# Kernel tuning notes

Measured on AMD Instinct MI355X. Metric: run time of the kernel, lower is better.

The kernel has to match this reference:

```python
import jax, jax.numpy as jnp
import numpy as np

ANCHORS_ALL = np.array([[10.,13.],[16.,30.],[33.,23.],[30.,61.],[62.,45.],
                        [59.,119.],[116.,90.],[156.,198.],[373.,326.]], np.float32)
ANCHORS_MASK = [0, 1, 2]
NUM_CLASS = 80
BBOX_ATTRIB = 5 + NUM_CLASS
IGNORE_THRES = 0.7
EPS = 1e-12


def _iou_cxcywh(a, b):
    ax1, ax2 = a[..., 0] - a[..., 2] / 2, a[..., 0] + a[..., 2] / 2
    ay1, ay2 = a[..., 1] - a[..., 3] / 2, a[..., 1] + a[..., 3] / 2
    bx1, bx2 = b[..., 0] - b[..., 2] / 2, b[..., 0] + b[..., 2] / 2
    by1, by2 = b[..., 1] - b[..., 3] / 2, b[..., 1] + b[..., 3] / 2
    iw = jnp.clip(jnp.minimum(ax2, bx2) - jnp.maximum(ax1, bx1), 0.0)
    ih = jnp.clip(jnp.minimum(ay2, by2) - jnp.maximum(ay1, by1), 0.0)
    inter = iw * ih
    union = a[..., 2] * a[..., 3] + b[..., 2] * b[..., 3] - inter
    return inter / (union + 1e-16)


def _build_targets(pred_boxes, target, anchors_all, anchors, nH, nW):
    # vectorized version of the per-(batch, gt-box) python double loop
    nB, nT, _ = target.shape
    nA = anchors.shape[0]
    # emulate `break` on first all-zero target row via cumulative validity
    valid = jnp.cumprod((target.sum(-1) != 0).astype(jnp.int32), axis=1).astype(bool)  # [B,T]
    gx, gy = target[..., 1] * nW, target[..., 2] * nH
    gw, gh = target[..., 3] * nW, target[..., 4] * nH
    gi = jnp.clip(gx.astype(jnp.int32), 0, nW - 1)
    gj = jnp.clip(gy.astype(jnp.int32), 0, nH - 1)
    gt_boxes = jnp.stack([gx, gy, gw, gh], -1)                                    # [B,T,4]
    # IoU of every GT against every predicted box -> ignore mask for noobj
    ious = _iou_cxcywh(pred_boxes.reshape(nB, 1, -1, 4), gt_boxes[:, :, None, :])  # [B,T,P]
    ignore = (ious > IGNORE_THRES) & valid[..., None]
    noobj_mask = 1.0 - jnp.any(ignore, axis=1).reshape(nB, nA, nH, nW).astype(jnp.float32)
    # anchor matching on w/h only (both boxes centered at origin)
    aw, ah = anchors_all[:, 0], anchors_all[:, 1]                                  # [9]
    inter = jnp.minimum(gw[..., None], aw) * jnp.minimum(gh[..., None], ah)
    union = gw[..., None] * gh[..., None] + aw * ah - inter
    best = jnp.argmax(inter / (union + 1e-16), axis=-1)                            # [B,T]
    lut = -np.ones(len(ANCHORS_ALL), np.int32)
    lut[np.array(ANCHORS_MASK)] = np.arange(nA, dtype=np.int32)
    a_loc = jnp.asarray(lut)[best]
    write = valid & (a_loc >= 0)                # only GTs whose best anchor is in this head's mask
    a_loc = jnp.clip(a_loc, 0)
    b_idx = jnp.where(write, jnp.arange(nB)[:, None], nB)   # route masked-out writes to dummy row nB
    coord_v = jnp.sqrt(2.0 - target[..., 3] * target[..., 4])
    tw_v = jnp.log(gw / anchors[a_loc, 0] + 1e-16)
    th_v = jnp.log(gh / anchors[a_loc, 1] + 1e-16)
    cls_i = jnp.clip(target[..., 0].astype(jnp.int32), 0, NUM_CLASS - 1)

    def scat(vals):
        return jnp.zeros((nB + 1, nA, nH, nW), jnp.float32).at[b_idx, a_loc, gj, gi].set(vals)[:nB]

    obj_mask = scat(jnp.ones_like(gx))
    box_coord_mask = scat(coord_v)
    tx = scat(gx - gi)
    ty = scat(gy - gj)
    tw = scat(tw_v)
    th = scat(th_v)
    tcls = (jnp.zeros((nB + 1, nA, nH, nW, NUM_CLASS), jnp.float32)
            .at[b_idx, a_loc, gj, gi, cls_i].set(1.0)[:nB])
    return obj_mask, noobj_mask, box_coord_mask, obj_mask, tcls, tx, ty, tw, th


def _bce_sum(p, t):
    return -jnp.sum(t * jnp.log(p + EPS) + (1.0 - t) * jnp.log(1.0 - p + EPS))


def _forward(x, target, img_dim):
    nB, _, nH, nW = x.shape
    nA = len(ANCHORS_MASK)
    stride = img_dim / nH
    anchors_all = jnp.asarray(ANCHORS_ALL) / stride
    anchors = anchors_all[jnp.asarray(ANCHORS_MASK)]
    preds = x.reshape(nB, nA, BBOX_ATTRIB, nH, nW).transpose(0, 1, 3, 4, 2)  # [B,A,H,W,85]
    preds_xy = jax.nn.sigmoid(preds[..., :2])
    preds_wh = preds[..., 2:4]
    preds_conf = jax.nn.sigmoid(preds[..., 4])
    preds_cls = jax.nn.sigmoid(preds[..., 5:])
    mesh_xy = jnp.stack(jnp.meshgrid(jnp.arange(nW, dtype=jnp.float32),
                                     jnp.arange(nH, dtype=jnp.float32)), -1)  # [H,W,2] = (x,y)
    # decoded boxes are detached in the original (used only to build targets)
    pred_boxes = jnp.concatenate(
        [jax.lax.stop_gradient(preds_xy) + mesh_xy,
         jnp.exp(jax.lax.stop_gradient(preds_wh)) * anchors[None, :, None, None, :]], -1)
    tgt = jax.lax.stop_gradient(target)  # target.detach() in original
    (obj_mask, noobj_mask, box_coord_mask, tconf, tcls,
     tx, ty, tw, th) = _build_targets(pred_boxes, tgt, anchors_all, anchors, nH, nW)
    mse = lambda a, b: jnp.sum((a - b) ** 2)
    loss_x = mse(preds_xy[..., 0] * box_coord_mask, tx * box_coord_mask) / 2
    loss_y = mse(preds_xy[..., 1] * box_coord_mask, ty * box_coord_mask) / 2
    loss_w = mse(preds_wh[..., 0] * box_coord_mask, tw * box_coord_mask) / 2
    loss_h = mse(preds_wh[..., 1] * box_coord_mask, th * box_coord_mask) / 2
    loss_conf = (_bce_sum(preds_conf * obj_mask, obj_mask)
                 + _bce_sum(preds_conf * noobj_mask, jnp.zeros_like(preds_conf)))
    # BCE over cls entries of object cells only (sum reduction) == mask-weighted sum
    loss_cls = -jnp.sum(obj_mask[..., None] * (tcls * jnp.log(preds_cls + EPS)
                                               + (1.0 - tcls) * jnp.log(1.0 - preds_cls + EPS)))
    return loss_x + loss_y + loss_w + loss_h + loss_conf + loss_cls


def setup_inputs() -> dict:
    key = jax.random.key(0)
    k1, k2, k3, k4 = jax.random.split(key, 4)
    nB, nT = 16, 50
    x = jax.random.normal(k1, (nB, 3 * BBOX_ATTRIB, 76, 76), jnp.float32)
    cls = jnp.floor(jax.random.uniform(k2, (nB, nT, 1)) * NUM_CLASS)
    cxy = jax.random.uniform(k3, (nB, nT, 2), minval=0.05, maxval=0.95)
    wh = jax.random.uniform(k4, (nB, nT, 2), minval=0.02, maxval=0.4)
    target = jnp.concatenate([cls, cxy, wh], -1).astype(jnp.float32)
    return {"x": x, "target": target, "img_dim": 608}


def reference(x, target, img_dim):
    return _forward(x, target, img_dim)
```

## Files before the change

kernel.cpp:

```cpp
#include <hip/hip_runtime.h>

#define NBATCH 16
#define NTGT   50
#define NA     3
#define NH     76
#define NW     76
#define HW     (NH*NW)
#define NC     80
#define NATT   85
#define CELLS  (NA*HW)

__device__ __constant__ float c_anchors[18] = {
  10.f,13.f, 16.f,30.f, 33.f,23.f, 30.f,61.f, 62.f,45.f,
  59.f,119.f, 116.f,90.f, 156.f,198.f, 373.f,326.f };

#define OFF_GX   0
#define OFF_GY   800
#define OFF_GW   1600
#define OFF_GH   2400
#define OFF_TX   3200
#define OFF_TY   4000
#define OFF_TW   4800
#define OFF_TH   5600
#define OFF_CV   6400
#define OFF_WKEY 7200
#define OFF_CLS  8000
#define OFF_NV   8800

__device__ inline float read_dim(const void* p) {
  int iv = *(const int*)p;
  if (iv > 0 && iv < (1 << 24)) return (float)iv;
  return *(const float*)p;
}

__global__ void yolo_prep(const float* __restrict__ tgt,
                          const void*  __restrict__ dimp,
                          float*       __restrict__ wsf) {
  int tid = threadIdx.x;
  int* wsi = (int*)wsf;
  if (tid < NBATCH) wsi[OFF_NV + tid] = NTGT;
  __syncthreads();
  if (tid < NBATCH * NTGT) {
    float stride = read_dim(dimp) / (float)NH;
    float inv_stride = 1.0f / stride;
    int b = tid / NTGT;
    const float* tr = tgt + tid * 5;
    float cls = tr[0], cx = tr[1], cy = tr[2], w = tr[3], h = tr[4];
    float s = cls + cx + cy + w + h;
    if (s == 0.0f) atomicMin(&wsi[OFF_NV + b], tid - b * NTGT);
    float gx = cx * NW, gy = cy * NH, gw = w * NW, gh = h * NH;
    int gi = min(max((int)gx, 0), NW - 1);
    int gj = min(max((int)gy, 0), NH - 1);
    float best_r = -1.0f; int best = 0;
    for (int k = 0; k < 9; k++) {
      float aw = c_anchors[2*k] * inv_stride, ah = c_anchors[2*k+1] * inv_stride;
      float inter = fminf(gw, aw) * fminf(gh, ah);
      float uni   = gw * gh + aw * ah - inter;
      float r = inter / (uni + 1e-16f);
      if (r > best_r) { best_r = r; best = k; }
    }
    int a_loc = (best < NA) ? best : 0;
    int wkey  = (best < NA) ? (a_loc * HW + gj * NW + gi) : -1;
    float aw = c_anchors[2*a_loc] * inv_stride, ah = c_anchors[2*a_loc+1] * inv_stride;
    wsf[OFF_GX + tid] = gx;  wsf[OFF_GY + tid] = gy;
    wsf[OFF_GW + tid] = gw;  wsf[OFF_GH + tid] = gh;
    wsf[OFF_TX + tid] = gx - (float)gi;
    wsf[OFF_TY + tid] = gy - (float)gj;
    wsf[OFF_TW + tid] = logf(gw / aw + 1e-16f);
    wsf[OFF_TH + tid] = logf(gh / ah + 1e-16f);
    wsf[OFF_CV + tid] = sqrtf(2.0f - w * h);
    int ci = (int)cls; ci = min(max(ci, 0), NC - 1);
    wsi[OFF_WKEY + tid] = wkey;
    wsi[OFF_CLS  + tid] = ci;
  }
}

__launch_bounds__(256)
__global__ void yolo_main(const float* __restrict__ x,
                          const float* __restrict__ wsf,
                          const void*  __restrict__ dimp,
                          float*       __restrict__ out) {
  __shared__ float sx1[NTGT], sx2[NTGT], sy1[NTGT], sy2[NTGT], sarea[NTGT];
  __shared__ float stx[NTGT], sty[NTGT], stw[NTGT], sth[NTGT], scv[NTGT];
  __shared__ int   swkey[NTGT], scls[NTGT];
  __shared__ int   snv;
  __shared__ float sred[4];

  int b   = blockIdx.y;
  int tid = threadIdx.x;
  if (tid < NTGT) {
    int g = b * NTGT + tid;
    float gx = wsf[OFF_GX+g], gy = wsf[OFF_GY+g], gw = wsf[OFF_GW+g], gh = wsf[OFF_GH+g];
    sx1[tid] = gx - gw * 0.5f;  sx2[tid] = gx + gw * 0.5f;
    sy1[tid] = gy - gh * 0.5f;  sy2[tid] = gy + gh * 0.5f;
    sarea[tid] = gw * gh;
    stx[tid] = wsf[OFF_TX+g];  sty[tid] = wsf[OFF_TY+g];
    stw[tid] = wsf[OFF_TW+g];  sth[tid] = wsf[OFF_TH+g];
    scv[tid] = wsf[OFF_CV+g];
    const int* wsi = (const int*)wsf;
    swkey[tid] = wsi[OFF_WKEY+g];
    scls[tid]  = wsi[OFF_CLS +g];
  }
  if (tid == 0) snv = ((const int*)wsf)[OFF_NV + b];
  __syncthreads();

  float loss = 0.0f;
  int cell = blockIdx.x * blockDim.x + tid;
  if (cell < CELLS) {
    int a   = cell / HW;
    int rem = cell - a * HW;
    int j   = rem / NW;
    int i   = rem - j * NW;
    const float* xb = x + (size_t)(b * (NA*NATT) + a * NATT) * HW + rem;
    float px = xb[0*HW], py = xb[1*HW], pw = xb[2*HW], ph = xb[3*HW], pc = xb[4*HW];
    float spx   = 1.0f / (1.0f + __expf(-px));
    float spy   = 1.0f / (1.0f + __expf(-py));
    float sconf = 1.0f / (1.0f + __expf(-pc));
    float stride = read_dim(dimp) / (float)NH;
    float aw = c_anchors[2*a] / stride, ah = c_anchors[2*a+1] / stride;
    float bw = __expf(pw) * aw, bh = __expf(ph) * ah;
    float bx = spx + (float)i, by = spy + (float)j;
    float ax1 = bx - bw * 0.5f, ax2 = bx + bw * 0.5f;
    float ay1 = by - bh * 0.5f, ay2 = by + bh * 0.5f;
    float areaA = bw * bh;

    int winner = -1;
    unsigned cb0 = 0, cb1 = 0, cb2 = 0;
    bool ign = false;
    int nv = snv;
    for (int t = 0; t < nv; t++) {
      float iw = fmaxf(fminf(ax2, sx2[t]) - fmaxf(ax1, sx1[t]), 0.0f);
      float ih = fmaxf(fminf(ay2, sy2[t]) - fmaxf(ay1, sy1[t]), 0.0f);
      float inter = iw * ih;
      float iou = inter / (areaA + sarea[t] - inter + 1e-16f);
      ign = ign | (iou > 0.7f);
      if (swkey[t] == cell) {
        winner = t;
        int c = scls[t];
        if (c < 32)      cb0 |= (1u << c);
        else if (c < 64) cb1 |= (1u << (c - 32));
        else             cb2 |= (1u << (c - 64));
      }
    }
    if (!ign) loss += -__logf(1.0f - sconf + 1e-12f);
    if (winner >= 0) {
      loss += -__logf(sconf + 1e-12f);
      float m  = scv[winner];
      float dx = (spx - stx[winner]) * m;
      float dy = (spy - sty[winner]) * m;
      float dw = (pw  - stw[winner]) * m;
      float dh = (ph  - sth[winner]) * m;
      loss += 0.5f * (dx*dx + dy*dy + dw*dw + dh*dh);
      for (int c = 0; c < NC; c++) {
        float pv = 1.0f / (1.0f + __expf(-xb[(5 + c) * HW]));
        bool on = (c < 32) ? ((cb0 >> c) & 1u)
                : (c < 64) ? ((cb1 >> (c - 32)) & 1u)
                           : ((cb2 >> (c - 64)) & 1u);
        loss += on ? -__logf(pv + 1e-12f) : -__logf(1.0f - pv + 1e-12f);
      }
    }
  }

  for (int off = 32; off > 0; off >>= 1) loss += __shfl_down(loss, off, 64);
  int wave = tid >> 6, lane = tid & 63;
  if (lane == 0) sred[wave] = loss;
  __syncthreads();
  if (tid == 0) {
    atomicAdd(out, sred[0] + sred[1] + sred[2] + sred[3]);
  }
}

extern "C" void kernel_launch(void* const* d_in, const int* in_sizes, int n_in,
                              void* d_out, int out_size, void* d_ws, size_t ws_size,
                              hipStream_t stream) {
  const float* x    = (const float*)d_in[0];
  const float* tgt  = (const float*)d_in[1];
  const void*  dimp = d_in[2];
  float* out = (float*)d_out;
  float* wsf = (float*)d_ws;

  hipMemsetAsync(out, 0, sizeof(float) * out_size, stream);

  yolo_prep<<<1, 832, 0, stream>>>(tgt, dimp, wsf);

  dim3 grid((CELLS + 255) / 256, NBATCH);
  yolo_main<<<grid, 256, 0, stream>>>(x, wsf, dimp, out);
}
```

Before: 170.1 us.

## Move object-cell loss into per-batch prep kernel; slim noobj IoU loop

Object-cell loss (box regression and class BCE) now runs in the prep kernel, one thread per GT. Duplicate keys are resolved so that the last GT with a given key wins and class bits are ORed. The per-cell main kernel keeps only the ignore-IoU test and reads packed float4 boxes from shared memory. The division is replaced by a multiply-compare, and the key comparison and bitmask work per cell per target are gone. This reduces the inner-loop instruction count and shared-memory traffic in the main kernel. In exchange, the prep kernel now does the serial 80-class loop for matched targets.

```diff
diff --git a/kernel.cpp b/kernel.cpp
--- a/kernel.cpp
+++ b/kernel.cpp
@@ -14,18 +14,8 @@
   10.f,13.f, 16.f,30.f, 33.f,23.f, 30.f,61.f, 62.f,45.f,
   59.f,119.f, 116.f,90.f, 156.f,198.f, 373.f,326.f };
 
-#define OFF_GX   0
-#define OFF_GY   800
-#define OFF_GW   1600
-#define OFF_GH   2400
-#define OFF_TX   3200
-#define OFF_TY   4000
-#define OFF_TW   4800
-#define OFF_TH   5600
-#define OFF_CV   6400
-#define OFF_WKEY 7200
-#define OFF_CLS  8000
-#define OFF_NV   8800
+#define OFF_AREA 3200
+#define OFF_NV   4000
 
 __device__ inline float read_dim(const void* p) {
   int iv = *(const int*)p;
@@ -33,73 +23,107 @@
   return *(const float*)p;
 }
 
-__global__ void yolo_prep(const float* __restrict__ tgt,
-                          const void*  __restrict__ dimp,
-                          float*       __restrict__ wsf) {
-  int tid = threadIdx.x;
-  int* wsi = (int*)wsf;
-  if (tid < NBATCH) wsi[OFF_NV + tid] = NTGT;
+__global__ void yolo_prep_obj(const float* __restrict__ tgt,
+                              const float* __restrict__ x,
+                              const void*  __restrict__ dimp,
+                              float*       __restrict__ wsf,
+                              float*       __restrict__ out) {
+  __shared__ int skey[NTGT];
+  __shared__ int scl [NTGT];
+  int b = blockIdx.x;
+  int t = threadIdx.x;
+  float istride = (float)NH / read_dim(dimp);
+
+  float cls = 0.f, cx = 0.f, cy = 0.f, w = 0.f, h = 0.f, s = 1.f;
+  if (t < NTGT) {
+    const float* tr = tgt + (size_t)(b * NTGT + t) * 5;
+    cls = tr[0]; cx = tr[1]; cy = tr[2]; w = tr[3]; h = tr[4];
+    s = cls + cx + cy + w + h;
+  }
+  unsigned long long mz = __ballot(t < NTGT && s == 0.0f);
+  int nv = mz ? (__ffsll(mz) - 1) : NTGT;
+
+  float gx = cx * NW, gy = cy * NH, gw = w * NW, gh = h * NH;
+  int gi = min(max((int)gx, 0), NW - 1);
+  int gj = min(max((int)gy, 0), NH - 1);
+
+  float best_r = -1.0f; int best = 0;
+  for (int k = 0; k < 9; k++) {
+    float aw = c_anchors[2*k] * istride, ah = c_anchors[2*k+1] * istride;
+    float inter = fminf(gw, aw) * fminf(gh, ah);
+    float uni   = gw * gh + aw * ah - inter;
+    float r = inter / (uni + 1e-16f);
+    if (r > best_r) { best_r = r; best = k; }
+  }
+  int a = (best < NA) ? best : 0;
+  int mykey = (t < nv && best < NA) ? (a * HW + gj * NW + gi) : -1;
+
+  if (t < NTGT) {
+    skey[t] = mykey;
+    scl [t] = min(max((int)cls, 0), NC - 1);
+    float4* wbox = (float4*)wsf;
+    wbox[b * NTGT + t] = make_float4(gx - gw*0.5f, gx + gw*0.5f,
+                                     gy - gh*0.5f, gy + gh*0.5f);
+    wsf[OFF_AREA + b * NTGT + t] = gw * gh;
+  }
+  if (t == 0) ((int*)wsf)[OFF_NV + b] = nv;
   __syncthreads();
-  if (tid < NBATCH * NTGT) {
-    float stride = read_dim(dimp) / (float)NH;
-    float inv_stride = 1.0f / stride;
-    int b = tid / NTGT;
-    const float* tr = tgt + tid * 5;
-    float cls = tr[0], cx = tr[1], cy = tr[2], w = tr[3], h = tr[4];
-    float s = cls + cx + cy + w + h;
-    if (s == 0.0f) atomicMin(&wsi[OFF_NV + b], tid - b * NTGT);
-    float gx = cx * NW, gy = cy * NH, gw = w * NW, gh = h * NH;
-    int gi = min(max((int)gx, 0), NW - 1);
-    int gj = min(max((int)gy, 0), NH - 1);
-    float best_r = -1.0f; int best = 0;
-    for (int k = 0; k < 9; k++) {
-      float aw = c_anchors[2*k] * inv_stride, ah = c_anchors[2*k+1] * inv_stride;
-      float inter = fminf(gw, aw) * fminf(gh, ah);
-      float uni   = gw * gh + aw * ah - inter;
-      float r = inter / (uni + 1e-16f);
-      if (r > best_r) { best_r = r; best = k; }
+
+  float loss = 0.0f;
+  if (mykey >= 0) {
+    bool winner = true;
+    unsigned cb0 = 0, cb1 = 0, cb2 = 0;
+    for (int t2 = 0; t2 < nv; t2++) {
+      if (skey[t2] == mykey) {
+        if (t2 > t) winner = false;
+        int c = scl[t2];
+        if (c < 32)      cb0 |= (1u << c);
+        else if (c < 64) cb1 |= (1u << (c - 32));
+        else             cb2 |= (1u << (c - 64));
+      }
     }
-    int a_loc = (best < NA) ? best : 0;
-    int wkey  = (best < NA) ? (a_loc * HW + gj * NW + gi) : -1;
-    float aw = c_anchors[2*a_loc] * inv_stride, ah = c_anchors[2*a_loc+1] * inv_stride;
-    wsf[OFF_GX + tid] = gx;  wsf[OFF_GY + tid] = gy;
-    wsf[OFF_GW + tid] = gw;  wsf[OFF_GH + tid] = gh;
-    wsf[OFF_TX + tid] = gx - (float)gi;
-    wsf[OFF_TY + tid] = gy - (float)gj;
-    wsf[OFF_TW + tid] = logf(gw / aw + 1e-16f);
-    wsf[OFF_TH + tid] = logf(gh / ah + 1e-16f);
-    wsf[OFF_CV + tid] = sqrtf(2.0f - w * h);
-    int ci = (int)cls; ci = min(max(ci, 0), NC - 1);
-    wsi[OFF_WKEY + tid] = wkey;
-    wsi[OFF_CLS  + tid] = ci;
+    if (winner) {
+      const float* xb = x + ((size_t)(b * NA + a) * NATT) * HW + gj * NW + gi;
+      float px = xb[0*HW], py = xb[1*HW], pw = xb[2*HW], ph = xb[3*HW], pc = xb[4*HW];
+      float spx   = 1.0f / (1.0f + __expf(-px));
+      float spy   = 1.0f / (1.0f + __expf(-py));
+      float sconf = 1.0f / (1.0f + __expf(-pc));
+      float aw = c_anchors[2*a] * istride, ah = c_anchors[2*a+1] * istride;
+      loss += -__logf(sconf + 1e-12f);
+      float m  = sqrtf(2.0f - w * h);
+      float dx = (spx - (gx - (float)gi)) * m;
+      float dy = (spy - (gy - (float)gj)) * m;
+      float dw = (pw  - __logf(gw / aw + 1e-16f)) * m;
+      float dh = (ph  - __logf(gh / ah + 1e-16f)) * m;
+      loss += 0.5f * (dx*dx + dy*dy + dw*dw + dh*dh);
+      for (int c = 0; c < NC; c++) {
+        float pv = 1.0f / (1.0f + __expf(-xb[(5 + c) * HW]));
+        bool on = (c < 32) ? ((cb0 >> c) & 1u)
+                : (c < 64) ? ((cb1 >> (c - 32)) & 1u)
+                           : ((cb2 >> (c - 64)) & 1u);
+        loss += on ? -__logf(pv + 1e-12f) : -__logf(1.0f - pv + 1e-12f);
+      }
+    }
   }
+  for (int off = 32; off > 0; off >>= 1) loss += __shfl_down(loss, off, 64);
+  if (t == 0) atomicAdd(out, loss);
 }
 
 __launch_bounds__(256)
-__global__ void yolo_main(const float* __restrict__ x,
-                          const float* __restrict__ wsf,
-                          const void*  __restrict__ dimp,
-                          float*       __restrict__ out) {
-  __shared__ float sx1[NTGT], sx2[NTGT], sy1[NTGT], sy2[NTGT], sarea[NTGT];
-  __shared__ float stx[NTGT], sty[NTGT], stw[NTGT], sth[NTGT], scv[NTGT];
-  __shared__ int   swkey[NTGT], scls[NTGT];
-  __shared__ int   snv;
-  __shared__ float sred[4];
+__global__ void yolo_noobj(const float* __restrict__ x,
+                           const float* __restrict__ wsf,
+                           const void*  __restrict__ dimp,
+                           float*       __restrict__ out) {
+  __shared__ float4 sbox[NTGT];
+  __shared__ float  sarea[NTGT];
+  __shared__ int    snv;
+  __shared__ float  sred[4];
 
   int b   = blockIdx.y;
   int tid = threadIdx.x;
   if (tid < NTGT) {
-    int g = b * NTGT + tid;
-    float gx = wsf[OFF_GX+g], gy = wsf[OFF_GY+g], gw = wsf[OFF_GW+g], gh = wsf[OFF_GH+g];
-    sx1[tid] = gx - gw * 0.5f;  sx2[tid] = gx + gw * 0.5f;
-    sy1[tid] = gy - gh * 0.5f;  sy2[tid] = gy + gh * 0.5f;
-    sarea[tid] = gw * gh;
-    stx[tid] = wsf[OFF_TX+g];  sty[tid] = wsf[OFF_TY+g];
-    stw[tid] = wsf[OFF_TW+g];  sth[tid] = wsf[OFF_TH+g];
-    scv[tid] = wsf[OFF_CV+g];
-    const int* wsi = (const int*)wsf;
-    swkey[tid] = wsi[OFF_WKEY+g];
-    scls[tid]  = wsi[OFF_CLS +g];
+    sbox [tid] = ((const float4*)wsf)[b * NTGT + tid];
+    sarea[tid] = wsf[OFF_AREA + b * NTGT + tid];
   }
   if (tid == 0) snv = ((const int*)wsf)[OFF_NV + b];
   __syncthreads();
@@ -111,63 +135,37 @@
     int rem = cell - a * HW;
     int j   = rem / NW;
     int i   = rem - j * NW;
-    const float* xb = x + (size_t)(b * (NA*NATT) + a * NATT) * HW + rem;
+    const float* xb = x + ((size_t)(b * NA + a) * NATT) * HW + rem;
     float px = xb[0*HW], py = xb[1*HW], pw = xb[2*HW], ph = xb[3*HW], pc = xb[4*HW];
     float spx   = 1.0f / (1.0f + __expf(-px));
     float spy   = 1.0f / (1.0f + __expf(-py));
     float sconf = 1.0f / (1.0f + __expf(-pc));
-    float stride = read_dim(dimp) / (float)NH;
-    float aw = c_anchors[2*a] / stride, ah = c_anchors[2*a+1] / stride;
-    float bw = __expf(pw) * aw, bh = __expf(ph) * ah;
+    float istride = (float)NH / read_dim(dimp);
+    float bw = __expf(pw) * c_anchors[2*a]   * istride;
+    float bh = __expf(ph) * c_anchors[2*a+1] * istride;
     float bx = spx + (float)i, by = spy + (float)j;
     float ax1 = bx - bw * 0.5f, ax2 = bx + bw * 0.5f;
     float ay1 = by - bh * 0.5f, ay2 = by + bh * 0.5f;
     float areaA = bw * bh;
 
-    int winner = -1;
-    unsigned cb0 = 0, cb1 = 0, cb2 = 0;
     bool ign = false;
     int nv = snv;
     for (int t = 0; t < nv; t++) {
-      float iw = fmaxf(fminf(ax2, sx2[t]) - fmaxf(ax1, sx1[t]), 0.0f);
-      float ih = fmaxf(fminf(ay2, sy2[t]) - fmaxf(ay1, sy1[t]), 0.0f);
+      float4 bb = sbox[t];
+      float iw = fmaxf(fminf(ax2, bb.y) - fmaxf(ax1, bb.x), 0.0f);
+      float ih = fmaxf(fminf(ay2, bb.w) - fmaxf(ay1, bb.z), 0.0f);
       float inter = iw * ih;
-      float iou = inter / (areaA + sarea[t] - inter + 1e-16f);
-      ign = ign | (iou > 0.7f);
-      if (swkey[t] == cell) {
-        winner = t;
-        int c = scls[t];
-        if (c < 32)      cb0 |= (1u << c);
-        else if (c < 64) cb1 |= (1u << (c - 32));
-        else             cb2 |= (1u << (c - 64));
-      }
+      float uni   = areaA + sarea[t] - inter + 1e-16f;
+      ign = ign | (inter > 0.7f * uni);
     }
     if (!ign) loss += -__logf(1.0f - sconf + 1e-12f);
-    if (winner >= 0) {
-      loss += -__logf(sconf + 1e-12f);
-      float m  = scv[winner];
-      float dx = (spx - stx[winner]) * m;
-      float dy = (spy - sty[winner]) * m;
-      float dw = (pw  - stw[winner]) * m;
-      float dh = (ph  - sth[winner]) * m;
-      loss += 0.5f * (dx*dx + dy*dy + dw*dw + dh*dh);
-      for (int c = 0; c < NC; c++) {
-        float pv = 1.0f / (1.0f + __expf(-xb[(5 + c) * HW]));
-        bool on = (c < 32) ? ((cb0 >> c) & 1u)
-                : (c < 64) ? ((cb1 >> (c - 32)) & 1u)
-                           : ((cb2 >> (c - 64)) & 1u);
-        loss += on ? -__logf(pv + 1e-12f) : -__logf(1.0f - pv + 1e-12f);
-      }
-    }
   }
 
   for (int off = 32; off > 0; off >>= 1) loss += __shfl_down(loss, off, 64);
   int wave = tid >> 6, lane = tid & 63;
   if (lane == 0) sred[wave] = loss;
   __syncthreads();
-  if (tid == 0) {
-    atomicAdd(out, sred[0] + sred[1] + sred[2] + sred[3]);
-  }
+  if (tid == 0) atomicAdd(out, sred[0] + sred[1] + sred[2] + sred[3]);
 }
 
 extern "C" void kernel_launch(void* const* d_in, const int* in_sizes, int n_in,
@@ -181,8 +179,8 @@
 
   hipMemsetAsync(out, 0, sizeof(float) * out_size, stream);
 
-  yolo_prep<<<1, 832, 0, stream>>>(tgt, dimp, wsf);
+  yolo_prep_obj<<<NBATCH, 64, 0, stream>>>(tgt, x, dimp, wsf, out);
 
   dim3 grid((CELLS + 255) / 256, NBATCH);
-  yolo_main<<<grid, 256, 0, stream>>>(x, wsf, dimp, out);
+  yolo_noobj<<<grid, 256, 0, stream>>>(x, wsf, dimp, out);
 }
```

Result: no change. 167.7 us (-1.4%).
